# Kernel optimization log

Hardware: AMD Instinct MI355X
Metric: run time of the kernel (lower is better)

The kernel has to match this reference:

```python
import jax, jax.numpy as jnp
import numpy as np

D_MODEL, D_HEAD, N_HEADS, D_LATENT, D_ROPE = 2048, 128, 16, 512, 64
ROPE_BASE = 10000.0
SCALE = 1.0 / np.sqrt(D_HEAD + D_ROPE)


def _rope(x):
    # x: [B, H, T, d_rope]; GPT-NeoX style half-split rotary
    T, d = x.shape[-2], x.shape[-1]
    inv_freq = 1.0 / (ROPE_BASE ** (jnp.arange(0, d, 2, dtype=jnp.float32) / d))
    ang = jnp.arange(T, dtype=jnp.float32)[:, None] * inv_freq[None, :]  # [T, d/2]
    cos = jnp.concatenate([jnp.cos(ang), jnp.cos(ang)], axis=-1)  # [T, d]
    sin = jnp.concatenate([jnp.sin(ang), jnp.sin(ang)], axis=-1)
    x1, x2 = x[..., : d // 2], x[..., d // 2 :]
    rot = jnp.concatenate([-x2, x1], axis=-1)
    return x * cos + rot * sin


def setup_inputs() -> dict:
    key = jax.random.key(0)
    ks = jax.random.split(key, 8)
    B, T = 2, 2048
    s = 0.02
    inp = {
        "x": jax.random.normal(ks[0], (B, T, D_MODEL), jnp.float32),
        "w_q": jax.random.normal(ks[1], (D_MODEL, D_MODEL), jnp.float32) * s,
        "w_dkv": jax.random.normal(ks[2], (D_LATENT, D_MODEL), jnp.float32) * s,
        "w_ukv": jax.random.normal(ks[3], (2 * D_MODEL, D_LATENT), jnp.float32) * s,
        "w_o": jax.random.normal(ks[4], (D_MODEL, D_MODEL), jnp.float32) * s,
        "w_q_rot": jax.random.normal(ks[5], (N_HEADS * D_ROPE, D_MODEL), jnp.float32) * s,
        "w_k_rot": jax.random.normal(ks[6], (D_ROPE, D_MODEL), jnp.float32) * s,
        "mask": jnp.triu(jnp.ones((T, T), dtype=bool), 1),  # True = blocked (causal)
    }
    return inp


def reference(x, w_q, w_dkv, w_ukv, w_o, w_q_rot, w_k_rot, mask):
    B, T, _ = x.shape
    # content queries  [B, H, T, d_head]
    q = (x @ w_q.T).reshape(B, T, N_HEADS, D_HEAD).transpose(0, 2, 1, 3)
    # latent KV compression -> expansion
    dkv = x @ w_dkv.T                       # [B, T, d_latent]
    ukv = (dkv @ w_ukv.T).reshape(B, T, N_HEADS, 2 * D_HEAD).transpose(0, 2, 1, 3)
    k, v = ukv[..., :D_HEAD], ukv[..., D_HEAD:]
    # decoupled rope parts
    q_rot = (x @ w_q_rot.T).reshape(B, T, N_HEADS, D_ROPE).transpose(0, 2, 1, 3)
    k_rot = jnp.broadcast_to((x @ w_k_rot.T)[:, None, :, :], (B, N_HEADS, T, D_ROPE))
    q = jnp.concatenate([q, _rope(q_rot)], axis=-1)   # [B, H, T, d_head+d_rope]
    k = jnp.concatenate([k, _rope(k_rot)], axis=-1)
    # SDPA with True-means-blocked mask
    scores = jnp.einsum("bhqd,bhkd->bhqk", q, k) * SCALE
    scores = jnp.where(mask, -jnp.inf, scores)
    attn = jax.nn.softmax(scores, axis=-1)
    out = jnp.einsum("bhqk,bhkd->bhqd", attn, v)      # [B, H, T, d_head]
    out = out.transpose(0, 2, 1, 3).reshape(B, T, D_MODEL)
    return out @ w_o.T
```

## Files before the change

kernel.cpp:

```cpp
#include <hip/hip_runtime.h>
#include <hip/hip_bf16.h>
#include <math.h>

#define T_SEQ 2048
#define QSTR  3648

typedef __bf16 bf16x8 __attribute__((ext_vector_type(8)));
typedef float  f32x4  __attribute__((ext_vector_type(4)));
typedef float  f32x16 __attribute__((ext_vector_type(16)));
typedef unsigned int u32x4 __attribute__((ext_vector_type(4)));

#define GLOAD_LDS16(g, l) __builtin_amdgcn_global_load_lds( \
    (const __attribute__((address_space(1))) void*)(g),      \
    (__attribute__((address_space(3))) void*)(l), 16, 0, 0)

#define VMCNT(n) asm volatile("s_waitcnt vmcnt(" #n ")" ::: "memory")

static __device__ __forceinline__ unsigned cvtpk_bf16(float a, float b)
{
    unsigned r;
    asm("v_cvt_pk_bf16_f32 %0, %1, %2" : "=v"(r) : "v"(a), "v"(b));
    return r;
}

static __device__ __forceinline__ float fexp2(float x)
{
    float r;
    asm("v_exp_f32 %0, %1" : "=v"(r) : "v"(x));
    return r;
}

struct CastArgs {
    const float* s[7];
    __bf16*      d[7];
    unsigned     cum[8];
};

__global__ __launch_bounds__(256) void cast_all(CastArgs a)
{
    const unsigned blk = blockIdx.x;
    int idx = 0;
    #pragma unroll
    for (int i = 1; i < 7; i++) if (blk >= a.cum[i]) idx = i;
    const unsigned local = blk - a.cum[idx];
    const float* src = a.s[idx];
    __bf16* dst = a.d[idx];
    const int i = (int)(local * 256 + threadIdx.x) * 8;
    float4 va = *reinterpret_cast<const float4*>(src + i);
    float4 vb = *reinterpret_cast<const float4*>(src + i + 4);
    bf16x8 f;
    f[0] = (__bf16)va.x; f[1] = (__bf16)va.y; f[2] = (__bf16)va.z; f[3] = (__bf16)va.w;
    f[4] = (__bf16)vb.x; f[5] = (__bf16)vb.y; f[6] = (__bf16)vb.z; f[7] = (__bf16)vb.w;
    *reinterpret_cast<bf16x8*>(dst + i) = f;
}

__global__ __launch_bounds__(256) void rope_all(__bf16* qcat)
{
    const unsigned blk = blockIdx.x;
    __bf16* buf;
    int shift, gid;
    if (blk < 8192) { buf = qcat + 2048; shift = 9; gid = blk * 256 + threadIdx.x; }
    else            { buf = qcat + 3072; shift = 5; gid = (blk - 8192) * 256 + threadIdx.x; }
    int row = gid >> shift;
    int rem = gid & ((1 << shift) - 1);
    int hb = rem >> 5, j = rem & 31;
    int t = row & (T_SEQ - 1);
    const float L2B = 0.4152410118609203f;
    float freq = exp2f(-L2B * (float)j);
    float sn, cs;
    __sincosf((float)t * freq, &sn, &cs);
    size_t base = (size_t)row * QSTR + hb * 64 + j;
    float v1 = (float)buf[base], v2 = (float)buf[base + 32];
    buf[base]      = (__bf16)(v1 * cs - v2 * sn);
    buf[base + 32] = (__bf16)(v2 * cs + v1 * sn);
}

__global__ __launch_bounds__(256) void prep_v(const __bf16* __restrict__ ukv,
                                              __bf16* __restrict__ vtt)
{
    __shared__ __align__(16) __bf16 Ls[64 * 136];
    const int tid = threadIdx.x;
    const int u = blockIdx.x, bh = blockIdx.y;
    const int b = bh >> 4, h = bh & 15;
    const size_t base = (size_t)b * T_SEQ + u * 64;
    #pragma unroll
    for (int p = 0; p < 4; p++) {
        int c = tid + 256 * p;
        int k = c >> 4, dv8 = (c & 15) * 8;
        *reinterpret_cast<bf16x8*>(Ls + k * 136 + dv8) =
            *reinterpret_cast<const bf16x8*>(ukv + (base + k) * 4096 + h * 256 + 128 + dv8);
    }
    __syncthreads();
    #pragma unroll
    for (int p = 0; p < 4; p++) {
        int c = tid + 256 * p;
        int dv = c >> 3, kb = c & 7;
        bf16x8 f;
        #pragma unroll
        for (int i = 0; i < 8; i++) f[i] = Ls[(kb * 8 + i) * 136 + dv];
        *reinterpret_cast<bf16x8*>(vtt + (((size_t)bh * 32 + u) * 128 + dv) * 64
                                   + ((kb ^ (dv & 7)) << 3)) = f;
    }
}

template <typename OutT>
__global__ __launch_bounds__(512, 2) void gemm_bt_256(const __bf16* __restrict__ A,
                                                      int lda,
                                                      const __bf16* __restrict__ B,
                                                      OutT* __restrict__ C,
                                                      int M, int N, int K)
{
    __shared__ __align__(16) __bf16 S[2 * 32768];
    const int tid  = threadIdx.x;
    const int lane = tid & 63;
    const int w    = tid >> 6;
    const int l15  = lane & 15, quad = lane >> 4;
    const int wm = w >> 2, wn = w & 3;
    const unsigned nwg = gridDim.x * gridDim.y;
    const unsigned fid = blockIdx.y * gridDim.x + blockIdx.x;
    const unsigned swz = (fid & 7) * (nwg >> 3) + (fid >> 3);
    const int m0 = (int)(swz / gridDim.x) * 256, n0 = (int)(swz % gridDim.x) * 256;
    const int NT = K >> 6;

    f32x4 acc[8][4] = {};
    bf16x8 af[4][2], bfr[2][2];

    auto stageA = [&](int T1, int h) {
        int d = T1 & 1;
        #pragma unroll
        for (int i = 0; i < 2; i++) {
            int c = i * 512 + tid;
            int lr = c >> 3, seg = c & 7;
            int g = ((lr >> 6) << 7) + h * 64 + (lr & 63);
            GLOAD_LDS16(A + (size_t)(m0 + g) * lda + T1 * 64 + ((seg ^ (lr & 7)) << 3),
                        S + d * 32768 + h * 8192 + c * 8);
        }
    };
    auto stageB = [&](int T1, int h) {
        int d = T1 & 1;
        #pragma unroll
        for (int i = 0; i < 2; i++) {
            int c = i * 512 + tid;
            int lr = c >> 3, seg = c & 7;
            int g = n0 + ((lr >> 5) << 6) + h * 32 + (lr & 31);
            if (g >= N) g = N - 1;
            GLOAD_LDS16(B + (size_t)g * K + T1 * 64 + ((seg ^ (lr & 7)) << 3),
                        S + d * 32768 + 16384 + h * 8192 + c * 8);
        }
    };

#define LOADA(d, mh) do {                                                      \
    const __bf16* Ah_ = S + (d) * 32768 + (mh) * 8192;                         \
    _Pragma("unroll")                                                          \
    for (int mi = 0; mi < 4; mi++) {                                           \
        int lr = wm * 64 + mi * 16 + l15;                                      \
        _Pragma("unroll")                                                      \
        for (int kk = 0; kk < 2; kk++)                                         \
            af[mi][kk] = *reinterpret_cast<const bf16x8*>(                     \
                Ah_ + lr * 64 + (((kk * 4 + quad) ^ (lr & 7)) << 3));          \
    }                                                                          \
} while (0)

#define LOADB(d, nh) do {                                                      \
    const __bf16* Bh_ = S + (d) * 32768 + 16384 + (nh) * 8192;                 \
    _Pragma("unroll")                                                          \
    for (int ni = 0; ni < 2; ni++) {                                           \
        int lr = wn * 32 + ni * 16 + l15;                                      \
        _Pragma("unroll")                                                      \
        for (int kk = 0; kk < 2; kk++)                                         \
            bfr[ni][kk] = *reinterpret_cast<const bf16x8*>(                    \
                Bh_ + lr * 64 + (((kk * 4 + quad) ^ (lr & 7)) << 3));          \
    }                                                                          \
} while (0)

#define SEAL() do {                                                            \
    __builtin_amdgcn_s_barrier();                                              \
    asm volatile("s_waitcnt lgkmcnt(0)" ::: "memory");                         \
    __builtin_amdgcn_sched_barrier(0);                                         \
} while (0)

#define MMA(mh, nh) do {                                                       \
    __builtin_amdgcn_s_setprio(1);                                             \
    _Pragma("unroll")                                                          \
    for (int mi = 0; mi < 4; mi++)                                             \
        _Pragma("unroll")                                                      \
        for (int ni = 0; ni < 2; ni++)                                         \
            _Pragma("unroll")                                                  \
            for (int kk = 0; kk < 2; kk++)                                     \
                acc[(mh) * 4 + mi][(nh) * 2 + ni] =                            \
                    __builtin_amdgcn_mfma_f32_16x16x32_bf16(                   \
                        af[mi][kk], bfr[ni][kk],                               \
                        acc[(mh) * 4 + mi][(nh) * 2 + ni], 0, 0, 0);           \
    __builtin_amdgcn_s_setprio(0);                                             \
} while (0)

    stageA(0, 0); stageB(0, 0); stageB(0, 1); stageA(0, 1);
    VMCNT(4);
    __builtin_amdgcn_s_barrier();

    for (int T = 0; T < NT - 1; T++) {
        const int d = T & 1;
        LOADA(d, 0); LOADB(d, 0); stageA(T + 1, 0); VMCNT(4); SEAL(); MMA(0, 0);
        LOADB(d, 1);              stageB(T + 1, 0); VMCNT(4); SEAL(); MMA(0, 1);
        LOADA(d, 1);              stageB(T + 1, 1);           SEAL(); MMA(1, 1);
        LOADB(d, 0);              stageA(T + 1, 1); VMCNT(4); SEAL(); MMA(1, 0);
    }
    {
        const int d = (NT - 1) & 1;
        LOADA(d, 0); LOADB(d, 0); VMCNT(2); SEAL(); MMA(0, 0);
        LOADB(d, 1);              VMCNT(0); SEAL(); MMA(0, 1);
        LOADA(d, 1);                        SEAL(); MMA(1, 1);
        LOADB(d, 0);                        SEAL(); MMA(1, 0);
    }
#undef LOADA
#undef LOADB
#undef SEAL
#undef MMA

    #pragma unroll
    for (int ai = 0; ai < 8; ai++) {
        #pragma unroll
        for (int bj = 0; bj < 4; bj++) {
            int col = n0 + wn * 64 + bj * 16 + l15;
            if (col < N) {
                #pragma unroll
                for (int r = 0; r < 4; r++) {
                    size_t row = m0 + wm * 128 + ai * 16 + quad * 4 + r;
                    C[row * (size_t)N + col] = (OutT)acc[ai][bj][r];
                }
            }
        }
    }
}

template <typename OutT>
__global__ __launch_bounds__(512) void gemm_bt_8ph(const __bf16* __restrict__ A,
                                                   int lda,
                                                   const __bf16* __restrict__ B,
                                                   OutT* __restrict__ C,
                                                   int M, int N, int K)
{
    __shared__ __align__(16) __bf16 S[2 * 24576];
    const int tid  = threadIdx.x;
    const int lane = tid & 63;
    const int w    = tid >> 6;
    const int l15  = lane & 15, quad = lane >> 4;
    const int wm = w >> 2, wn = w & 3;
    const unsigned nwg = gridDim.x * gridDim.y;
    const unsigned fid = blockIdx.y * gridDim.x + blockIdx.x;
    const unsigned swz = (fid & 7) * (nwg >> 3) + (fid >> 3);
    const int m0 = (int)(swz / gridDim.x) * 128, n0 = (int)(swz % gridDim.x) * 256;
    const int NT = K >> 6;

    f32x4 acc[4][4] = {};

    const int lrA = tid >> 3, segA = tid & 7;

    auto stageA = [&](int T1, int h) {
        int d = T1 & 1;
        int g = ((lrA >> 5) << 6) + h * 32 + (lrA & 31);
        GLOAD_LDS16(A + (size_t)(m0 + g) * lda + T1 * 64 + ((segA ^ (lrA & 7)) << 3),
                    S + d * 24576 + h * 4096 + tid * 8);
    };
    auto stageB = [&](int T1, int h) {
        int d = T1 & 1;
        #pragma unroll
        for (int i = 0; i < 2; i++) {
            int c = i * 512 + tid;
            int lr = c >> 3, seg = c & 7;
            int g = n0 + ((lr >> 5) << 6) + h * 32 + (lr & 31);
            if (g >= N) g = N - 1;
            GLOAD_LDS16(B + (size_t)g * K + T1 * 64 + ((seg ^ (lr & 7)) << 3),
                        S + d * 24576 + 8192 + h * 8192 + c * 8);
        }
    };

#define PHASE(d, mh, nh, STAGE, WAIT) do {                                     \
    const __bf16* Ah_ = S + (d) * 24576 + (mh) * 4096;                         \
    const __bf16* Bh_ = S + (d) * 24576 + 8192 + (nh) * 8192;                  \
    bf16x8 af[2][2], bfr[2][2];                                                \
    _Pragma("unroll")                                                          \
    for (int mr = 0; mr < 2; mr++) {                                           \
        int ar = wm * 32 + mr * 16 + l15;                                      \
        _Pragma("unroll")                                                      \
        for (int kk = 0; kk < 2; kk++)                                         \
            af[mr][kk] = *reinterpret_cast<const bf16x8*>(                     \
                Ah_ + ar * 64 + (((kk * 4 + quad) ^ (ar & 7)) << 3));          \
    }                                                                          \
    _Pragma("unroll")                                                          \
    for (int nr = 0; nr < 2; nr++) {                                           \
        int br = wn * 32 + nr * 16 + l15;                                      \
        _Pragma("unroll")                                                      \
        for (int kk = 0; kk < 2; kk++)                                         \
            bfr[nr][kk] = *reinterpret_cast<const bf16x8*>(                    \
                Bh_ + br * 64 + (((kk * 4 + quad) ^ (br & 7)) << 3));          \
    }                                                                          \
    STAGE;                                                                     \
    WAIT;                                                                      \
    __builtin_amdgcn_s_barrier();                                              \
    asm volatile("s_waitcnt lgkmcnt(0)" ::: "memory");                         \
    __builtin_amdgcn_sched_barrier(0);                                         \
    __builtin_amdgcn_s_setprio(1);                                             \
    _Pragma("unroll")                                                          \
    for (int mr = 0; mr < 2; mr++)                                             \
        _Pragma("unroll")                                                      \
        for (int nr = 0; nr < 2; nr++)                                         \
            _Pragma("unroll")                                                  \
            for (int kk = 0; kk < 2; kk++)                                     \
                acc[(mh) * 2 + mr][(nh) * 2 + nr] =                            \
                    __builtin_amdgcn_mfma_f32_16x16x32_bf16(                   \
                        af[mr][kk], bfr[nr][kk],                               \
                        acc[(mh) * 2 + mr][(nh) * 2 + nr], 0, 0, 0);           \
    __builtin_amdgcn_s_setprio(0);                                             \
} while (0)

    stageA(0, 0);
    stageB(0, 0);
    stageB(0, 1);
    stageA(0, 1);
    VMCNT(3);
    __builtin_amdgcn_s_barrier();

    for (int T = 0; T < NT - 1; T++) {
        const int d = T & 1;
        PHASE(d, 0, 0, stageA(T + 1, 0), VMCNT(2));
        PHASE(d, 0, 1, stageB(T + 1, 0), VMCNT(3));
        PHASE(d, 1, 0, stageB(T + 1, 1), (void)0);
        PHASE(d, 1, 1, stageA(T + 1, 1), VMCNT(3));
    }
    {
        const int d = (NT - 1) & 1;
        PHASE(d, 0, 0, (void)0, VMCNT(1));
        PHASE(d, 0, 1, (void)0, VMCNT(0));
        PHASE(d, 1, 0, (void)0, (void)0);
        PHASE(d, 1, 1, (void)0, (void)0);
    }
#undef PHASE

    #pragma unroll
    for (int ai = 0; ai < 4; ai++) {
        #pragma unroll
        for (int bj = 0; bj < 4; bj++) {
            int col = n0 + wn * 64 + bj * 16 + l15;
            if (col < N) {
                #pragma unroll
                for (int r = 0; r < 4; r++) {
                    size_t row = m0 + wm * 64 + ai * 16 + quad * 4 + r;
                    C[row * (size_t)N + col] = (OutT)acc[ai][bj][r];
                }
            }
        }
    }
}

__global__ __launch_bounds__(256, 2) void flash_mfma(
    const __bf16* __restrict__ qcat, const __bf16* __restrict__ ukv,
    const __bf16* __restrict__ vtt, __bf16* __restrict__ obuf)
{
    __shared__ __align__(16) __bf16 LDS[40960];

    const int tid  = threadIdx.x;
    const int w    = tid >> 6;
    const int lane = tid & 63;
    const int l31  = lane & 31;
    const int lh   = lane >> 5;
    const int l15  = lane & 15;
    const int quad = lane >> 4;
    const int gx = blockIdx.x, gy = blockIdx.y;
    int bh, qi;
    if (gy < 16) { bh = gy * 2;            qi = gx; }
    else         { bh = (gy - 16) * 2 + 1; qi = 15 - gx; }
    const int b = bh >> 4, h = bh & 15;
    const int q0 = qi * 128;
    const float SC2 = 0.10411754900f;
    const size_t urow = (size_t)b * T_SEQ;

    const int q = q0 + 32 * w + l31;
    bf16x8 qf[12];
    {
        const __bf16* qrow = qcat + (urow + q) * QSTR + h * 128;
        #pragma unroll
        for (int dk = 0; dk < 8; dk++)
            qf[dk] = *reinterpret_cast<const bf16x8*>(qrow + 16 * dk + 8 * lh);
        const __bf16* qrr = qcat + (urow + q) * QSTR + 2048 + h * 64;
        #pragma unroll
        for (int dk = 0; dk < 4; dk++)
            qf[8 + dk] = *reinterpret_cast<const bf16x8*>(qrr + 16 * dk + 8 * lh);
    }

    f32x16 o[4] = {};
    float m_i = -INFINITY, l_i = 0.f;

    const int nunits = 2 * qi + 2;

    auto stage = [&](int x) {
        const int d1 = x & 1;
        const size_t roff = urow + (size_t)64 * x;
        #pragma unroll
        for (int p = 0; p < 4; p++) {
            int c = tid + 256 * p;
            int row = c >> 4, seg = c & 15;
            GLOAD_LDS16(ukv + (roff + row) * 4096 + h * 256 + ((seg ^ (row & 7)) << 3),
                        LDS + d1 * 8192 + c * 8);
        }
        #pragma unroll
        for (int p = 0; p < 2; p++) {
            int c = tid + 256 * p;
            int row = c >> 3, seg = c & 7;
            GLOAD_LDS16(qcat + (roff + row) * QSTR + 3072 + ((seg ^ (row & 7)) << 3),
                        LDS + 16384 + d1 * 4096 + c * 8);
        }
        const __bf16* vsrc = vtt + ((size_t)bh * 32 + x) * 8192;
        #pragma unroll
        for (int p = 0; p < 4; p++) {
            int c = tid + 256 * p;
            GLOAD_LDS16(vsrc + c * 8, LDS + 24576 + d1 * 8192 + c * 8);
        }
    };

    stage(0);
    VMCNT(0);
    __builtin_amdgcn_s_barrier();

    for (int u = 0; u < nunits; u++) {
        if (u + 1 < nunits) { stage(u + 1); VMCNT(10); }
        else                { VMCNT(0); }
        __builtin_amdgcn_s_barrier();
        __builtin_amdgcn_sched_barrier(0);

        const int d1 = u & 1;
        const __bf16* KN = LDS + d1 * 8192;
        const __bf16* KR = LDS + 16384 + d1 * 4096;
        const __bf16* VT = LDS + 24576 + d1 * 8192;
        const int key = l31 & 7;
        const int k0 = 64 * u;
        const bool domask = (u + 2 >= nunits);

        f32x16 s2[2] = {};
        __builtin_amdgcn_s_setprio(1);
        #pragma unroll
        for (int t = 0; t < 2; t++) {
            const __bf16* kn = KN + (32 * t + l31) * 128;
            const __bf16* kr = KR + (32 * t + l31) * 64;
            #pragma unroll
            for (int dk = 0; dk < 8; dk++) {
                bf16x8 kf = *reinterpret_cast<const bf16x8*>(kn + (((2 * dk + lh) ^ key) << 3));
                s2[t] = __builtin_amdgcn_mfma_f32_32x32x16_bf16(kf, qf[dk], s2[t], 0, 0, 0);
            }
            #pragma unroll
            for (int dk = 0; dk < 4; dk++) {
                bf16x8 kf = *reinterpret_cast<const bf16x8*>(kr + (((2 * dk + lh) ^ key) << 3));
                s2[t] = __builtin_amdgcn_mfma_f32_32x32x16_bf16(kf, qf[8 + dk], s2[t], 0, 0, 0);
            }
        }
        __builtin_amdgcn_s_setprio(0);

        #pragma unroll
        for (int t = 0; t < 2; t++) {
            float rmax = -INFINITY;
            #pragma unroll
            for (int g = 0; g < 16; g++) {
                float v = s2[t][g] * SC2;
                if (domask) {
                    int kg = k0 + 32 * t + (g & 3) + 8 * (g >> 2) + 4 * lh;
                    if (kg > q) v = -INFINITY;
                }
                s2[t][g] = v;
                rmax = fmaxf(rmax, v);
            }
            rmax = fmaxf(rmax, __shfl_xor(rmax, 32, 64));
            if (__any(rmax > m_i + 8.0f)) {
                const float mnew  = fmaxf(m_i, rmax);
                const float alpha = fexp2(m_i - mnew);
                m_i = mnew;
                l_i *= alpha;
                #pragma unroll
                for (int dt = 0; dt < 4; dt++) o[dt] *= alpha;
            }
            float part = 0.f;
            #pragma unroll
            for (int g = 0; g < 16; g++) {
                float pv = fexp2(s2[t][g] - m_i);
                s2[t][g] = pv;
                part += pv;
            }
            l_i += part;

            __builtin_amdgcn_s_setprio(1);
            unsigned Ap[4], Bp[4];
            #pragma unroll
            for (int g = 0; g < 4; g++) {
                Ap[g] = cvtpk_bf16(s2[t][4 * g],     s2[t][4 * g + 1]);
                Bp[g] = cvtpk_bf16(s2[t][4 * g + 2], s2[t][4 * g + 3]);
            }
            #pragma unroll
            for (int sub = 0; sub < 2; sub++) {
                unsigned xA = lh ? Ap[2 * sub] : Ap[2 * sub + 1];
                unsigned xB = lh ? Bp[2 * sub] : Bp[2 * sub + 1];
                unsigned rA = __shfl_xor(xA, 32, 64);
                unsigned rB = __shfl_xor(xB, 32, 64);
                u32x4 uv;
                uv[0] = lh ? rA : Ap[2 * sub];
                uv[1] = lh ? rB : Bp[2 * sub];
                uv[2] = lh ? Ap[2 * sub + 1] : rA;
                uv[3] = lh ? Bp[2 * sub + 1] : rB;
                bf16x8 pf = __builtin_bit_cast(bf16x8, uv);
                const int s = 2 * t + sub;
                #pragma unroll
                for (int dt = 0; dt < 4; dt++) {
                    bf16x8 vf = *reinterpret_cast<const bf16x8*>(
                        VT + (32 * dt + l31) * 64 + (((2 * s + lh) ^ key) << 3));
                    o[dt] = __builtin_amdgcn_mfma_f32_32x32x16_bf16(vf, pf, o[dt], 0, 0, 0);
                }
            }
            __builtin_amdgcn_s_setprio(0);
        }

        __builtin_amdgcn_sched_barrier(0);
        __builtin_amdgcn_s_barrier();
    }

    const float linv = 1.0f / (l_i + __shfl_xor(l_i, 32, 64));
    float* Os = reinterpret_cast<float*>(LDS);
    #pragma unroll
    for (int dt = 0; dt < 4; dt++)
        #pragma unroll
        for (int g = 0; g < 16; g++) {
            int d = 32 * dt + (g & 3) + 8 * (g >> 2) + 4 * lh;
            Os[(32 * w + l31) * 132 + d] = o[dt][g] * linv;
        }
    asm volatile("s_waitcnt lgkmcnt(0)" ::: "memory");
    __builtin_amdgcn_sched_barrier(0);
    #pragma unroll
    for (int p = 0; p < 8; p++) {
        int row = 32 * w + 4 * p + quad;
        float4 a4 = *reinterpret_cast<const float4*>(Os + row * 132 + 8 * l15);
        float4 c2 = *reinterpret_cast<const float4*>(Os + row * 132 + 8 * l15 + 4);
        bf16x8 f;
        f[0] = (__bf16)a4.x; f[1] = (__bf16)a4.y; f[2] = (__bf16)a4.z; f[3] = (__bf16)a4.w;
        f[4] = (__bf16)c2.x; f[5] = (__bf16)c2.y; f[6] = (__bf16)c2.z; f[7] = (__bf16)c2.w;
        *reinterpret_cast<bf16x8*>(obuf + (urow + q0 + row) * 2048 + h * 128 + 8 * l15) = f;
    }
}

extern "C" void kernel_launch(void* const* d_in, const int* in_sizes, int n_in,
                              void* d_out, int out_size, void* d_ws, size_t ws_size,
                              hipStream_t stream)
{
    const float* x      = (const float*)d_in[0];
    const float* w_q    = (const float*)d_in[1];
    const float* w_dkv  = (const float*)d_in[2];
    const float* w_ukv  = (const float*)d_in[3];
    const float* w_o    = (const float*)d_in[4];
    const float* w_qrot = (const float*)d_in[5];
    const float* w_krot = (const float*)d_in[6];
    float* out = (float*)d_out;

    const size_t M = 4096;
    __bf16* ws   = (__bf16*)d_ws;
    __bf16* xb   = ws;
    __bf16* wcat = xb + M * 2048;
    __bf16* wqb  = wcat;
    __bf16* wqrb = wcat + (size_t)2048 * 2048;
    __bf16* wkrb = wqrb + (size_t)1024 * 2048;
    __bf16* wdkb = wkrb + (size_t)64 * 2048;
    __bf16* wukb = wcat + (size_t)QSTR * 2048;
    __bf16* wob  = wukb + (size_t)4096 * 512;
    __bf16* qcat = wob  + (size_t)2048 * 2048;
    __bf16* ukv  = qcat + M * QSTR;
    __bf16* ao   = ukv  + M * 4096;
    __bf16* vtt  = ao   + M * 2048;

    dim3 blk(256);

    CastArgs ca;
    ca.s[0] = x;      ca.d[0] = xb;
    ca.s[1] = w_q;    ca.d[1] = wqb;
    ca.s[2] = w_qrot; ca.d[2] = wqrb;
    ca.s[3] = w_krot; ca.d[3] = wkrb;
    ca.s[4] = w_dkv;  ca.d[4] = wdkb;
    ca.s[5] = w_ukv;  ca.d[5] = wukb;
    ca.s[6] = w_o;    ca.d[6] = wob;
    ca.cum[0] = 0;
    ca.cum[1] = ca.cum[0] + 4096;
    ca.cum[2] = ca.cum[1] + 2048;
    ca.cum[3] = ca.cum[2] + 1024;
    ca.cum[4] = ca.cum[3] + 64;
    ca.cum[5] = ca.cum[4] + 512;
    ca.cum[6] = ca.cum[5] + 1024;
    ca.cum[7] = ca.cum[6] + 2048;
    cast_all<<<ca.cum[7], blk, 0, stream>>>(ca);

    gemm_bt_256<__bf16><<<dim3(15, 16), dim3(512), 0, stream>>>(
        xb, 2048, wcat, qcat, 4096, QSTR, 2048);
    gemm_bt_256<__bf16><<<dim3(16, 16), dim3(512), 0, stream>>>(
        qcat + 3136, QSTR, wukb, ukv, 4096, 4096, 512);

    rope_all<<<8704, blk, 0, stream>>>(qcat);
    prep_v<<<dim3(32, 32), blk, 0, stream>>>(ukv, vtt);

    flash_mfma<<<dim3(16, 32), dim3(256), 0, stream>>>(qcat, ukv, vtt, ao);

    gemm_bt_8ph<float><<<dim3(8, 32), dim3(512), 0, stream>>>(
        ao, 2048, wob, out, 4096, 2048, 2048);
}
```

Before: 354.9 us.

## Snake-order GEMM phases to reuse fragments and merge flash softmax passes

The output-projection GEMM now visits its four quarter-tiles in snake order (00, 01, 11, 10) and keeps the A/B register fragments across phases, so each phase reloads only one operand from LDS instead of both. The epilogue column and row mapping is rewritten to match the new layout. Separately, the flash attention kernel computes the row max and online-softmax rescale once per 64-key unit instead of once per 32-key half, which removes one cross-lane shuffle, any-vote and rescale per unit. Keeping fragments live across phases raises register pressure in the GEMM.

```diff
diff --git a/kernel.cpp b/kernel.cpp
--- a/kernel.cpp
+++ b/kernel.cpp
@@ -234,11 +234,11 @@
 }
 
 template <typename OutT>
-__global__ __launch_bounds__(512) void gemm_bt_8ph(const __bf16* __restrict__ A,
-                                                   int lda,
-                                                   const __bf16* __restrict__ B,
-                                                   OutT* __restrict__ C,
-                                                   int M, int N, int K)
+__global__ __launch_bounds__(512) void gemm_bt_sn128(const __bf16* __restrict__ A,
+                                                     int lda,
+                                                     const __bf16* __restrict__ B,
+                                                     OutT* __restrict__ C,
+                                                     int M, int N, int K)
 {
     __shared__ __align__(16) __bf16 S[2 * 24576];
     const int tid  = threadIdx.x;
@@ -253,9 +253,9 @@
     const int NT = K >> 6;
 
     f32x4 acc[4][4] = {};
+    bf16x8 af[2][2], bfr[2][2];
 
     const int lrA = tid >> 3, segA = tid & 7;
-
     auto stageA = [&](int T1, int h) {
         int d = T1 & 1;
         int g = ((lrA >> 5) << 6) + h * 32 + (lrA & 31);
@@ -275,77 +275,86 @@
         }
     };
 
-#define PHASE(d, mh, nh, STAGE, WAIT) do {                                     \
+#define LOADAx(d, mh) do {                                                     \
     const __bf16* Ah_ = S + (d) * 24576 + (mh) * 4096;                         \
-    const __bf16* Bh_ = S + (d) * 24576 + 8192 + (nh) * 8192;                  \
-    bf16x8 af[2][2], bfr[2][2];                                                \
     _Pragma("unroll")                                                          \
-    for (int mr = 0; mr < 2; mr++) {                                           \
-        int ar = wm * 32 + mr * 16 + l15;                                      \
+    for (int mi = 0; mi < 2; mi++) {                                           \
+        int lr = wm * 32 + mi * 16 + l15;                                      \
         _Pragma("unroll")                                                      \
         for (int kk = 0; kk < 2; kk++)                                         \
-            af[mr][kk] = *reinterpret_cast<const bf16x8*>(                     \
-                Ah_ + ar * 64 + (((kk * 4 + quad) ^ (ar & 7)) << 3));          \
+            af[mi][kk] = *reinterpret_cast<const bf16x8*>(                     \
+                Ah_ + lr * 64 + (((kk * 4 + quad) ^ (lr & 7)) << 3));          \
     }                                                                          \
+} while (0)
+
+#define LOADBx(d, nh) do {                                                     \
+    const __bf16* Bh_ = S + (d) * 24576 + 8192 + (nh) * 8192;                  \
     _Pragma("unroll")                                                          \
-    for (int nr = 0; nr < 2; nr++) {                                           \
-        int br = wn * 32 + nr * 16 + l15;                                      \
+    for (int ni = 0; ni < 2; ni++) {                                           \
+        int lr = wn * 32 + ni * 16 + l15;                                      \
         _Pragma("unroll")                                                      \
         for (int kk = 0; kk < 2; kk++)                                         \
-            bfr[nr][kk] = *reinterpret_cast<const bf16x8*>(                    \
-                Bh_ + br * 64 + (((kk * 4 + quad) ^ (br & 7)) << 3));          \
+            bfr[ni][kk] = *reinterpret_cast<const bf16x8*>(                    \
+                Bh_ + lr * 64 + (((kk * 4 + quad) ^ (lr & 7)) << 3));          \
     }                                                                          \
-    STAGE;                                                                     \
-    WAIT;                                                                      \
+} while (0)
+
+#define SEALx() do {                                                           \
     __builtin_amdgcn_s_barrier();                                              \
     asm volatile("s_waitcnt lgkmcnt(0)" ::: "memory");                         \
     __builtin_amdgcn_sched_barrier(0);                                         \
+} while (0)
+
+#define MMAx(mh, nh) do {                                                      \
     __builtin_amdgcn_s_setprio(1);                                             \
     _Pragma("unroll")                                                          \
-    for (int mr = 0; mr < 2; mr++)                                             \
+    for (int mi = 0; mi < 2; mi++)                                             \
         _Pragma("unroll")                                                      \
-        for (int nr = 0; nr < 2; nr++)                                         \
+        for (int ni = 0; ni < 2; ni++)                                         \
             _Pragma("unroll")                                                  \
             for (int kk = 0; kk < 2; kk++)                                     \
-                acc[(mh) * 2 + mr][(nh) * 2 + nr] =                            \
+                acc[(mh) * 2 + mi][(nh) * 2 + ni] =                            \
                     __builtin_amdgcn_mfma_f32_16x16x32_bf16(                   \
-                        af[mr][kk], bfr[nr][kk],                               \
-                        acc[(mh) * 2 + mr][(nh) * 2 + nr], 0, 0, 0);           \
+                        af[mi][kk], bfr[ni][kk],                               \
+                        acc[(mh) * 2 + mi][(nh) * 2 + ni], 0, 0, 0);           \
     __builtin_amdgcn_s_setprio(0);                                             \
 } while (0)
 
-    stageA(0, 0);
-    stageB(0, 0);
-    stageB(0, 1);
-    stageA(0, 1);
+    stageA(0, 0); stageB(0, 0); stageB(0, 1); stageA(0, 1);
     VMCNT(3);
     __builtin_amdgcn_s_barrier();
 
     for (int T = 0; T < NT - 1; T++) {
         const int d = T & 1;
-        PHASE(d, 0, 0, stageA(T + 1, 0), VMCNT(2));
-        PHASE(d, 0, 1, stageB(T + 1, 0), VMCNT(3));
-        PHASE(d, 1, 0, stageB(T + 1, 1), (void)0);
-        PHASE(d, 1, 1, stageA(T + 1, 1), VMCNT(3));
+        LOADAx(d, 0); LOADBx(d, 0); stageA(T + 1, 0); VMCNT(2); SEALx(); MMAx(0, 0);
+        LOADBx(d, 1);               stageB(T + 1, 0); VMCNT(3); SEALx(); MMAx(0, 1);
+        LOADAx(d, 1);               stageB(T + 1, 1);           SEALx(); MMAx(1, 1);
+        LOADBx(d, 0);               stageA(T + 1, 1); VMCNT(3); SEALx(); MMAx(1, 0);
     }
     {
         const int d = (NT - 1) & 1;
-        PHASE(d, 0, 0, (void)0, VMCNT(1));
-        PHASE(d, 0, 1, (void)0, VMCNT(0));
-        PHASE(d, 1, 0, (void)0, (void)0);
-        PHASE(d, 1, 1, (void)0, (void)0);
-    }
-#undef PHASE
+        LOADAx(d, 0); LOADBx(d, 0); VMCNT(1); SEALx(); MMAx(0, 0);
+        LOADBx(d, 1);               VMCNT(0); SEALx(); MMAx(0, 1);
+        LOADAx(d, 1);                         SEALx(); MMAx(1, 1);
+        LOADBx(d, 0);                         SEALx(); MMAx(1, 0);
+    }
+#undef LOADAx
+#undef LOADBx
+#undef SEALx
+#undef MMAx
 
     #pragma unroll
     for (int ai = 0; ai < 4; ai++) {
         #pragma unroll
         for (int bj = 0; bj < 4; bj++) {
-            int col = n0 + wn * 64 + bj * 16 + l15;
+            const int mh = ai >> 1, mi = ai & 1;
+            const int nh = bj >> 1, ni = bj & 1;
+            const int lrB = wn * 32 + ni * 16 + l15;
+            int col = n0 + ((lrB >> 5) << 6) + nh * 32 + (lrB & 31);
             if (col < N) {
                 #pragma unroll
                 for (int r = 0; r < 4; r++) {
-                    size_t row = m0 + wm * 64 + ai * 16 + quad * 4 + r;
+                    size_t row = m0 + wm * 64 + mh * 32 + mi * 16 + quad * 4 + r;
                     C[row * (size_t)N + col] = (OutT)acc[ai][bj][r];
                 }
             }
@@ -433,8 +442,6 @@
         const __bf16* KR = LDS + 16384 + d1 * 4096;
         const __bf16* VT = LDS + 24576 + d1 * 8192;
         const int key = l31 & 7;
-        const int k0 = 64 * u;
-        const bool domask = (u + 2 >= nunits);
 
         f32x16 s2[2] = {};
         __builtin_amdgcn_s_setprio(1);
@@ -455,9 +462,11 @@
         }
         __builtin_amdgcn_s_setprio(0);
 
-        #pragma unroll
-        for (int t = 0; t < 2; t++) {
-            float rmax = -INFINITY;
+        const int k0 = 64 * u;
+        const bool domask = (u + 2 >= nunits);
+        float rmax = -INFINITY;
+        #pragma unroll
+        for (int t = 0; t < 2; t++)
             #pragma unroll
             for (int g = 0; g < 16; g++) {
                 float v = s2[t][g] * SC2;
@@ -468,25 +477,29 @@
                 s2[t][g] = v;
                 rmax = fmaxf(rmax, v);
             }
-            rmax = fmaxf(rmax, __shfl_xor(rmax, 32, 64));
-            if (__any(rmax > m_i + 8.0f)) {
-                const float mnew  = fmaxf(m_i, rmax);
-                const float alpha = fexp2(m_i - mnew);
-                m_i = mnew;
-                l_i *= alpha;
-                #pragma unroll
-                for (int dt = 0; dt < 4; dt++) o[dt] *= alpha;
-            }
-            float part = 0.f;
+        rmax = fmaxf(rmax, __shfl_xor(rmax, 32, 64));
+        if (__any(rmax > m_i + 8.0f)) {
+            const float mnew  = fmaxf(m_i, rmax);
+            const float alpha = fexp2(m_i - mnew);
+            m_i = mnew;
+            l_i *= alpha;
+            #pragma unroll
+            for (int dt = 0; dt < 4; dt++) o[dt] *= alpha;
+        }
+        float part = 0.f;
+        #pragma unroll
+        for (int t = 0; t < 2; t++)
             #pragma unroll
             for (int g = 0; g < 16; g++) {
                 float pv = fexp2(s2[t][g] - m_i);
                 s2[t][g] = pv;
                 part += pv;
             }
-            l_i += part;
-
-            __builtin_amdgcn_s_setprio(1);
+        l_i += part;
+
+        __builtin_amdgcn_s_setprio(1);
+        #pragma unroll
+        for (int t = 0; t < 2; t++) {
             unsigned Ap[4], Bp[4];
             #pragma unroll
             for (int g = 0; g < 4; g++) {
@@ -513,8 +526,8 @@
                     o[dt] = __builtin_amdgcn_mfma_f32_32x32x16_bf16(vf, pf, o[dt], 0, 0, 0);
                 }
             }
-            __builtin_amdgcn_s_setprio(0);
-        }
+        }
+        __builtin_amdgcn_s_setprio(0);
 
         __builtin_amdgcn_sched_barrier(0);
         __builtin_amdgcn_s_barrier();
@@ -601,6 +614,6 @@
 
     flash_mfma<<<dim3(16, 32), dim3(256), 0, stream>>>(qcat, ukv, vtt, ao);
 
-    gemm_bt_8ph<float><<<dim3(8, 32), dim3(512), 0, stream>>>(
+    gemm_bt_sn128<float><<<dim3(8, 32), dim3(512), 0, stream>>>(
         ao, 2048, wob, out, 4096, 2048, 2048);
 }
```

Measured after the change: 351.9 us. Within noise of the previous version (-0.8%).
